# Kernel optimization log

Measured on AMD Instinct MI355X. Metric: run time of the kernel, lower is better.

Reference implementation:

```python
import jax, jax.numpy as jnp
import numpy as np
from jax import lax


def setup_inputs() -> dict:
    key = jax.random.key(0)
    kx, kk = jax.random.split(key)
    B, H, W, Cin, Cout, K = 32, 128, 128, 128, 128, 3
    X = jax.random.normal(kx, (B, H, W, Cin), dtype=jnp.float32)
    kernel = jax.random.normal(kk, (B, K, K, Cin, Cout), dtype=jnp.float32)
    return {"X": X, "kernel": kernel}


def reference(X, kernel):
    """Per-sample dynamic conv2d: each batch element gets its own HWIO kernel.

    Equivalent math to the TF depthwise-trick + reduce_sum, but expressed as a
    vmapped standard convolution (fuses the input-channel reduction, avoiding
    the huge [H',W',B*Cin,Cout] intermediate). Padding = 'VALID'.
    """
    dn = ('NHWC', 'HWIO', 'NHWC')

    def conv_one(x, k):
        # x: [H, W, Cin], k: [kh, kw, Cin, Cout] -> [H', W', Cout]
        return lax.conv_general_dilated(
            x[None], k, window_strides=(1, 1), padding='VALID',
            dimension_numbers=dn)[0]

    return jax.vmap(conv_one)(X, kernel)  # [B, H', W', Cout]
```

## Files before the change

### kernel.cpp

```cpp
#include <hip/hip_runtime.h>
#include <stdint.h>

typedef __attribute__((ext_vector_type(8))) short bf16x8;
typedef __attribute__((ext_vector_type(4))) float f32x4;
typedef __attribute__((ext_vector_type(4))) unsigned short u16x4;
typedef __attribute__((ext_vector_type(4))) unsigned int u32x4;

#define NB 32
#define HH 128
#define WW 128
#define CI 128
#define CO 128
#define HO 126
#define WO 126
#define TH 16
#define TW 16
#define PHh 18
#define PWw 18
#define NROW (PHh * PWw)
#define RSTR 72
#define RSTRB 144

__device__ __forceinline__ unsigned short f2bf(float f) {
  union { float f; unsigned u; } x; x.f = f;
  unsigned u = x.u;
  u += 0x7FFFu + ((u >> 16) & 1u);
  return (unsigned short)(u >> 16);
}

__device__ __forceinline__ unsigned cvtpk_bf16(float a, float b) {
  unsigned r;
  asm("v_cvt_pk_bf16_f32 %0, %1, %2" : "=v"(r) : "v"(a), "v"(b));
  return r;
}

__global__ void prep_kt(const float* __restrict__ kin, unsigned short* __restrict__ ktr) {
  __shared__ unsigned short t[CI * CO];
  int bp = blockIdx.x;
  int b = bp / 9, p = bp % 9;
  const float* src = kin + (size_t)bp * (CI * CO);
  unsigned short* dstb = ktr + (size_t)b * (9 * CI * CO);
  for (int i = threadIdx.x; i < CI * CO / 4; i += blockDim.x) {
    f32x4 v = *(const f32x4*)(src + i * 4);
    u16x4 o;
    o.x = f2bf(v.x); o.y = f2bf(v.y); o.z = f2bf(v.z); o.w = f2bf(v.w);
    *(u16x4*)&t[i * 4] = o;
  }
  __syncthreads();
  for (int j = threadIdx.x; j < 2048; j += blockDim.x) {
    int lane = j & 63, f = (j >> 6) & 7, sl = j >> 9;
    int ch = sl >> 1, kc = sl & 1;
    int co = (f >> 2) * 64 + (f & 3) * 16 + (lane & 15);
    int ci0 = ch * 64 + kc * 32 + (lane >> 4) * 8;
    bf16x8 v;
#pragma unroll
    for (int e = 0; e < 8; ++e) v[e] = t[(ci0 + e) * CO + co];
    int slice = (ch * 9 + p) * 2 + kc;
    *(bf16x8*)&dstb[(size_t)slice * 4096 + f * 512 + lane * 8] = v;
  }
}

__global__ void conv_naive(const float* __restrict__ X, const float* __restrict__ Kf,
                           float* __restrict__ out) {
  int idx = blockIdx.x * blockDim.x + threadIdx.x;
  if (idx >= NB * HO * WO * CO) return;
  int co = idx & 127, t = idx >> 7;
  int wp = t % WO; t /= WO;
  int hp = t % HO; int b = t / HO;
  const float* xb = X + (size_t)b * HH * WW * CI;
  const float* kb = Kf + (size_t)b * 9 * CI * CO;
  float s = 0.f;
  for (int p = 0; p < 9; ++p) {
    int kh = p / 3, kw = p % 3;
    const float* xr = xb + ((size_t)(hp + kh) * WW + (wp + kw)) * CI;
    const float* kr = kb + (size_t)p * CI * CO + co;
    for (int ci = 0; ci < CI; ++ci) s += xr[ci] * kr[(size_t)ci * CO];
  }
  out[idx] = s;
}

__global__ __launch_bounds__(512, 2) void conv_main(
    const float* __restrict__ X, const unsigned short* __restrict__ Kt,
    float* __restrict__ out) {
  __shared__ unsigned short lds_a[2][NROW * RSTR];

  const int tid = threadIdx.x;
  const int lane = tid & 63;
  const int wid = tid >> 6;
  const int wr = wid >> 2, wc = wid & 3;
  const int ks = lane >> 4, lr = lane & 15;

  const int bx = blockIdx.x;
  const int xcd = bx & 7, v = bx >> 3;
  const int b = xcd * 4 + (v >> 3);
  const int wt = v & 7;
  const int w0 = wt * TW;

  const float* xb = X + (size_t)b * HH * WW * CI;

  const int ci8 = tid & 7;
  unsigned okw = 0;
  int hI[6]; unsigned baseI[6];
#pragma unroll
  for (int i = 0; i < 6; ++i) {
    int row = (tid >> 3) + 64 * i;
    int h = row / PWw, w = row - PWw * h;
    int gw = w0 + w;
    if (gw < WW) okw |= (1u << i);
    hI[i] = h;
    baseI[i] = (unsigned)((h * WW + (gw & 127)) * CI + ci8 * 8);
  }
  const int dst0 = (tid >> 3) * RSTR + ci8 * 8;

  auto sIssue = [&](int i, int h0n, int chn, f32x4& ga, f32x4& gb) {
    bool live = (i < 5) | (tid < 32);
    bool ok = live && ((okw >> i) & 1) && (h0n + hI[i] < HH);
    const float* sp = xb + (ok ? baseI[i] + (unsigned)(h0n << 14) + (unsigned)(chn << 6)
                               : (unsigned)(ci8 << 3));
    ga = *(const f32x4*)sp;
    gb = *(const f32x4*)(sp + 4);
  };
  auto sWrite = [&](int i, int h0n, unsigned short* wbuf, const f32x4& ga, const f32x4& gb) {
    bool live = (i < 5) | (tid < 32);
    if (!live) return;
    bool ok = ((okw >> i) & 1) && (h0n + hI[i] < HH);
    u32x4 o;
    o.x = ok ? cvtpk_bf16(ga.x, ga.y) : 0u;
    o.y = ok ? cvtpk_bf16(ga.z, ga.w) : 0u;
    o.z = ok ? cvtpk_bf16(gb.x, gb.y) : 0u;
    o.w = ok ? cvtpk_bf16(gb.z, gb.w) : 0u;
    *(u32x4*)&wbuf[dst0 + i * 4608] = o;
  };

  const int aoff = ((wr * 8) * PWw + lr) * RSTRB + ks * 16;

  const unsigned short* ktw = Kt + (size_t)b * 9 * CI * CO + (wc * 2) * 512 + lane * 8;
  bf16x8 Hf[3][2];
  auto loadB = [&](bf16x8 (&dst)[2], const unsigned short* p) {
#pragma unroll
    for (int n = 0; n < 2; ++n)
      dst[n] = *(const bf16x8*)(p + n * 512);
  };

  f32x4 zero = {0.f, 0.f, 0.f, 0.f};
  f32x4 acc[8][2];
#pragma unroll
  for (int m = 0; m < 8; ++m)
#pragma unroll
    for (int n = 0; n < 2; ++n) acc[m][n] = zero;

  unsigned short* const A0 = &lds_a[0][0];
  unsigned short* const A1 = &lds_a[1][0];
  float* const ob = out + (size_t)b * HO * WO * CO;

  {
    f32x4 a0, b0, a1, b1, a2, b2;
    sIssue(0, 0, 0, a0, b0); sIssue(1, 0, 0, a1, b1); sIssue(2, 0, 0, a2, b2);
    sWrite(0, 0, A0, a0, b0); sWrite(1, 0, A0, a1, b1); sWrite(2, 0, A0, a2, b2);
    sIssue(3, 0, 0, a0, b0); sIssue(4, 0, 0, a1, b1); sIssue(5, 0, 0, a2, b2);
    sWrite(3, 0, A0, a0, b0); sWrite(4, 0, A0, a1, b1); sWrite(5, 0, A0, a2, b2);
  }
  loadB(Hf[0], ktw);
  loadB(Hf[1], ktw + 4096);
  __syncthreads();

  f32x4 g0a, g0b, g1a, g1b, g2a, g2b;

#pragma unroll 1
  for (int k = 0; k < 16; ++k) {
    const int ch = k & 1;
    const int h0 = (k >> 1) * TH;
    unsigned short* rbuf = ch ? A1 : A0;
    unsigned short* wbuf = ch ? A0 : A1;
    const unsigned short* bq = ktw + (size_t)ch * 73728;
    const bool stg = (k < 15);
    const int chn = (k + 1) & 1;
    const int h0n = ((k + 1) >> 1) * TH;
    const unsigned short* bqn = ktw + (size_t)chn * 73728;
    const char* rb = (const char*)rbuf;

#pragma unroll
    for (int s = 0; s < 18; ++s) {
      if (s < 16) loadB(Hf[(s + 2) % 3], bq + (size_t)(s + 2) * 4096);
      else if (stg) loadB(Hf[(s + 2) % 3], bqn + (size_t)(s - 16) * 4096);
      if (stg && s == 0) {
        sIssue(0, h0n, chn, g0a, g0b);
        sIssue(1, h0n, chn, g1a, g1b);
        sIssue(2, h0n, chn, g2a, g2b);
      }
      {
        const int kh = s / 6, jj = s % 6;
        const int kw = jj >> 1, kc = jj & 1;
        bf16x8 af[8];
#pragma unroll
        for (int m = 0; m < 8; ++m)
          af[m] = *(const bf16x8*)(rb + aoff +
                                   ((m + kh) * PWw * RSTRB + kw * RSTRB + kc * 64));
        __builtin_amdgcn_s_setprio(1);
#pragma unroll
        for (int m = 0; m < 8; ++m)
#pragma unroll
          for (int n = 0; n < 2; ++n)
            acc[m][n] = __builtin_amdgcn_mfma_f32_16x16x32_bf16(af[m], Hf[s % 3][n],
                                                                acc[m][n], 0, 0, 0);
        __builtin_amdgcn_s_setprio(0);
      }
      if (stg && s == 5) {
        sWrite(0, h0n, wbuf, g0a, g0b);
        sWrite(1, h0n, wbuf, g1a, g1b);
        sWrite(2, h0n, wbuf, g2a, g2b);
        sIssue(3, h0n, chn, g0a, g0b);
        sIssue(4, h0n, chn, g1a, g1b);
        sIssue(5, h0n, chn, g2a, g2b);
      }
      if (stg && s == 11) {
        sWrite(3, h0n, wbuf, g0a, g0b);
        sWrite(4, h0n, wbuf, g1a, g1b);
        sWrite(5, h0n, wbuf, g2a, g2b);
      }
    }

    if (ch) {
#pragma unroll
      for (int m = 0; m < 8; ++m) {
        int hp = h0 + wr * 8 + m;
        if (hp >= HO) continue;
#pragma unroll
        for (int r = 0; r < 4; ++r) {
          int wp = w0 + ks * 4 + r;
          if (wp >= WO) continue;
#pragma unroll
          for (int n = 0; n < 2; ++n) {
            int co = wc * 32 + n * 16 + lr;
            ob[((size_t)hp * WO + wp) * CO + co] = acc[m][n][r];
          }
        }
      }
#pragma unroll
      for (int m = 0; m < 8; ++m)
#pragma unroll
        for (int n = 0; n < 2; ++n) acc[m][n] = zero;
    }
    if (k < 15) __syncthreads();
  }
}

extern "C" void kernel_launch(void* const* d_in, const int* in_sizes, int n_in,
                              void* d_out, int out_size, void* d_ws, size_t ws_size,
                              hipStream_t stream) {
  const float* X = (const float*)d_in[0];
  const float* Kf = (const float*)d_in[1];
  float* out = (float*)d_out;
  size_t need = (size_t)NB * 9 * CI * CO * sizeof(unsigned short);
  if (d_ws != nullptr && ws_size >= need) {
    unsigned short* ktr = (unsigned short*)d_ws;
    prep_kt<<<dim3(NB * 9), 256, 0, stream>>>(Kf, ktr);
    conv_main<<<dim3(256), 512, 0, stream>>>(X, ktr, out);
  } else {
    int total = NB * HO * WO * CO;
    conv_naive<<<(total + 255) / 256, 256, 0, stream>>>(X, Kf, out);
  }
}
```

Before: 178.2 us.

## Enlarge row tile to 21 with 12 waves per block and re-pipeline staging

```diff
diff --git a/kernel.cpp b/kernel.cpp
--- a/kernel.cpp
+++ b/kernel.cpp
@@ -13,11 +13,11 @@
 #define CO 128
 #define HO 126
 #define WO 126
-#define TH 16
+#define TH3 21
 #define TW 16
-#define PHh 18
+#define PH3 23
 #define PWw 18
-#define NROW (PHh * PWw)
+#define NR3 (PH3 * PWw)
 #define RSTR 72
 #define RSTRB 144
 
@@ -79,10 +79,10 @@
   out[idx] = s;
 }
 
-__global__ __launch_bounds__(512, 2) void conv_main(
+__global__ __launch_bounds__(768, 3) void conv_main(
     const float* __restrict__ X, const unsigned short* __restrict__ Kt,
     float* __restrict__ out) {
-  __shared__ unsigned short lds_a[2][NROW * RSTR];
+  __shared__ unsigned short lds_a[2][NR3 * RSTR];
 
   const int tid = threadIdx.x;
   const int lane = tid & 63;
@@ -99,131 +99,120 @@
   const float* xb = X + (size_t)b * HH * WW * CI;
 
   const int ci8 = tid & 7;
-  unsigned okw = 0;
-  int hI[6]; unsigned baseI[6];
-#pragma unroll
-  for (int i = 0; i < 6; ++i) {
-    int row = (tid >> 3) + 64 * i;
-    int h = row / PWw, w = row - PWw * h;
-    int gw = w0 + w;
-    if (gw < WW) okw |= (1u << i);
-    hI[i] = h;
-    baseI[i] = (unsigned)((h * WW + (gw & 127)) * CI + ci8 * 8);
-  }
-  const int dst0 = (tid >> 3) * RSTR + ci8 * 8;
-
-  auto sIssue = [&](int i, int h0n, int chn, f32x4& ga, f32x4& gb) {
-    bool live = (i < 5) | (tid < 32);
-    bool ok = live && ((okw >> i) & 1) && (h0n + hI[i] < HH);
-    const float* sp = xb + (ok ? baseI[i] + (unsigned)(h0n << 14) + (unsigned)(chn << 6)
-                               : (unsigned)(ci8 << 3));
-    ga = *(const f32x4*)sp;
-    gb = *(const f32x4*)(sp + 4);
+  const int row0 = tid >> 3;
+  const int h00 = row0 / PWw, w00 = row0 - PWw * h00;
+  const int dst0 = row0 * RSTR + ci8 * 8;
+
+  const int aoff = ((wr * 7) * PWw + lr) * RSTRB + ks * 16;
+
+  const unsigned short* ktw = Kt + (size_t)b * 9 * CI * CO + (wc * 2) * 512 + lane * 8;
+  bf16x8 Hf[2][2];
+  auto loadB = [&](bf16x8 (&dst)[2], const unsigned short* p) {
+    dst[0] = *(const bf16x8*)(p);
+    dst[1] = *(const bf16x8*)(p + 512);
   };
-  auto sWrite = [&](int i, int h0n, unsigned short* wbuf, const f32x4& ga, const f32x4& gb) {
-    bool live = (i < 5) | (tid < 32);
-    if (!live) return;
-    bool ok = ((okw >> i) & 1) && (h0n + hI[i] < HH);
-    u32x4 o;
-    o.x = ok ? cvtpk_bf16(ga.x, ga.y) : 0u;
-    o.y = ok ? cvtpk_bf16(ga.z, ga.w) : 0u;
-    o.z = ok ? cvtpk_bf16(gb.x, gb.y) : 0u;
-    o.w = ok ? cvtpk_bf16(gb.z, gb.w) : 0u;
-    *(u32x4*)&wbuf[dst0 + i * 4608] = o;
-  };
-
-  const int aoff = ((wr * 8) * PWw + lr) * RSTRB + ks * 16;
-
-  const unsigned short* ktw = Kt + (size_t)b * 9 * CI * CO + (wc * 2) * 512 + lane * 8;
-  bf16x8 Hf[3][2];
-  auto loadB = [&](bf16x8 (&dst)[2], const unsigned short* p) {
-#pragma unroll
-    for (int n = 0; n < 2; ++n)
-      dst[n] = *(const bf16x8*)(p + n * 512);
-  };
 
   f32x4 zero = {0.f, 0.f, 0.f, 0.f};
-  f32x4 acc[8][2];
-#pragma unroll
-  for (int m = 0; m < 8; ++m)
+  f32x4 acc[7][2];
+#pragma unroll
+  for (int m = 0; m < 7; ++m)
 #pragma unroll
     for (int n = 0; n < 2; ++n) acc[m][n] = zero;
 
-  unsigned short* const A0 = &lds_a[0][0];
-  unsigned short* const A1 = &lds_a[1][0];
   float* const ob = out + (size_t)b * HO * WO * CO;
 
   {
-    f32x4 a0, b0, a1, b1, a2, b2;
-    sIssue(0, 0, 0, a0, b0); sIssue(1, 0, 0, a1, b1); sIssue(2, 0, 0, a2, b2);
-    sWrite(0, 0, A0, a0, b0); sWrite(1, 0, A0, a1, b1); sWrite(2, 0, A0, a2, b2);
-    sIssue(3, 0, 0, a0, b0); sIssue(4, 0, 0, a1, b1); sIssue(5, 0, 0, a2, b2);
-    sWrite(3, 0, A0, a0, b0); sWrite(4, 0, A0, a1, b1); sWrite(5, 0, A0, a2, b2);
+    int hC = h00, wC = w00;
+#pragma unroll
+    for (int g = 0; g < 5; ++g) {
+      bool live = (g < 4) | (tid < 240);
+      int gh = hC, gw = w0 + wC;
+      bool ok = live && ((gh | gw) < HH);
+      const float* sp = xb + ((size_t)(((gh & 127) << 7) + (gw & 127)) << 7) + ci8 * 8;
+      f32x4 ga = *(const f32x4*)sp;
+      f32x4 gb = *(const f32x4*)(sp + 4);
+      if (live) {
+        u32x4 o;
+        o.x = ok ? cvtpk_bf16(ga.x, ga.y) : 0u;
+        o.y = ok ? cvtpk_bf16(ga.z, ga.w) : 0u;
+        o.z = ok ? cvtpk_bf16(gb.x, gb.y) : 0u;
+        o.w = ok ? cvtpk_bf16(gb.z, gb.w) : 0u;
+        *(u32x4*)&lds_a[0][dst0 + g * 6912] = o;
+      }
+      wC += 6; if (wC >= PWw) { wC -= PWw; hC += 6; } else hC += 5;
+    }
   }
   loadB(Hf[0], ktw);
-  loadB(Hf[1], ktw + 4096);
   __syncthreads();
 
-  f32x4 g0a, g0b, g1a, g1b, g2a, g2b;
+  f32x4 gAa, gAb, gBa, gBb; bool okA = false, okB = false;
+  int hC = h00, wC = w00;
 
 #pragma unroll 1
-  for (int k = 0; k < 16; ++k) {
-    const int ch = k & 1;
-    const int h0 = (k >> 1) * TH;
-    unsigned short* rbuf = ch ? A1 : A0;
-    unsigned short* wbuf = ch ? A0 : A1;
+  for (int kp = 0; kp < 12; ++kp) {
+    const int ch = kp & 1;
+    const int h0 = (kp >> 1) * TH3;
+    const char* rb = (const char*)&lds_a[kp & 1][0];
+    unsigned short* wbuf = &lds_a[(kp + 1) & 1][0];
     const unsigned short* bq = ktw + (size_t)ch * 73728;
-    const bool stg = (k < 15);
-    const int chn = (k + 1) & 1;
-    const int h0n = ((k + 1) >> 1) * TH;
+    const bool stg = (kp < 11);
+    const int chn = (kp + 1) & 1;
+    const int h0n = ((kp + 1) >> 1) * TH3;
     const unsigned short* bqn = ktw + (size_t)chn * 73728;
-    const char* rb = (const char*)rbuf;
+    if (stg) { hC = h00; wC = w00; }
 
 #pragma unroll
     for (int s = 0; s < 18; ++s) {
-      if (s < 16) loadB(Hf[(s + 2) % 3], bq + (size_t)(s + 2) * 4096);
-      else if (stg) loadB(Hf[(s + 2) % 3], bqn + (size_t)(s - 16) * 4096);
-      if (stg && s == 0) {
-        sIssue(0, h0n, chn, g0a, g0b);
-        sIssue(1, h0n, chn, g1a, g1b);
-        sIssue(2, h0n, chn, g2a, g2b);
+      const int kh = s / 6, jj = s % 6;
+      const int kw = jj >> 1, kc = jj & 1;
+      if (s < 17) loadB(Hf[(s + 1) & 1], bq + (size_t)(s + 1) * 4096);
+      else if (stg) loadB(Hf[0], bqn);
+      if (stg && s >= 2 && s < 7) {
+        const int g = s - 2;
+        bool live = (g < 4) | (tid < 240);
+        if (live) {
+          bool ok = (g & 1) ? okB : okA;
+          f32x4 ga = (g & 1) ? gBa : gAa;
+          f32x4 gb = (g & 1) ? gBb : gAb;
+          u32x4 o;
+          o.x = ok ? cvtpk_bf16(ga.x, ga.y) : 0u;
+          o.y = ok ? cvtpk_bf16(ga.z, ga.w) : 0u;
+          o.z = ok ? cvtpk_bf16(gb.x, gb.y) : 0u;
+          o.w = ok ? cvtpk_bf16(gb.z, gb.w) : 0u;
+          *(u32x4*)&wbuf[dst0 + g * 6912] = o;
+        }
+      }
+      if (stg && s < 5) {
+        bool live = (s < 4) | (tid < 240);
+        int gh = h0n + hC, gw = w0 + wC;
+        bool ok = live && ((gh | gw) < HH);
+        const float* sp = xb + ((size_t)(((gh & 127) << 7) + (gw & 127)) << 7)
+                          + chn * 64 + ci8 * 8;
+        if (s & 1) { gBa = *(const f32x4*)sp; gBb = *(const f32x4*)(sp + 4); okB = ok; }
+        else       { gAa = *(const f32x4*)sp; gAb = *(const f32x4*)(sp + 4); okA = ok; }
+        wC += 6; if (wC >= PWw) { wC -= PWw; hC += 6; } else hC += 5;
       }
       {
-        const int kh = s / 6, jj = s % 6;
-        const int kw = jj >> 1, kc = jj & 1;
-        bf16x8 af[8];
-#pragma unroll
-        for (int m = 0; m < 8; ++m)
+        bf16x8 af[7];
+#pragma unroll
+        for (int m = 0; m < 7; ++m)
           af[m] = *(const bf16x8*)(rb + aoff +
-                                   ((m + kh) * PWw * RSTRB + kw * RSTRB + kc * 64));
+                                   (((m + kh) * PWw + kw) * RSTRB + kc * 64));
         __builtin_amdgcn_s_setprio(1);
 #pragma unroll
-        for (int m = 0; m < 8; ++m)
+        for (int m = 0; m < 7; ++m)
 #pragma unroll
           for (int n = 0; n < 2; ++n)
-            acc[m][n] = __builtin_amdgcn_mfma_f32_16x16x32_bf16(af[m], Hf[s % 3][n],
+            acc[m][n] = __builtin_amdgcn_mfma_f32_16x16x32_bf16(af[m], Hf[s & 1][n],
                                                                 acc[m][n], 0, 0, 0);
         __builtin_amdgcn_s_setprio(0);
       }
-      if (stg && s == 5) {
-        sWrite(0, h0n, wbuf, g0a, g0b);
-        sWrite(1, h0n, wbuf, g1a, g1b);
-        sWrite(2, h0n, wbuf, g2a, g2b);
-        sIssue(3, h0n, chn, g0a, g0b);
-        sIssue(4, h0n, chn, g1a, g1b);
-        sIssue(5, h0n, chn, g2a, g2b);
-      }
-      if (stg && s == 11) {
-        sWrite(3, h0n, wbuf, g0a, g0b);
-        sWrite(4, h0n, wbuf, g1a, g1b);
-        sWrite(5, h0n, wbuf, g2a, g2b);
-      }
     }
 
     if (ch) {
 #pragma unroll
-      for (int m = 0; m < 8; ++m) {
-        int hp = h0 + wr * 8 + m;
+      for (int m = 0; m < 7; ++m) {
+        int hp = h0 + wr * 7 + m;
         if (hp >= HO) continue;
 #pragma unroll
         for (int r = 0; r < 4; ++r) {
@@ -237,11 +226,11 @@
         }
       }
 #pragma unroll
-      for (int m = 0; m < 8; ++m)
+      for (int m = 0; m < 7; ++m)
 #pragma unroll
         for (int n = 0; n < 2; ++n) acc[m][n] = zero;
     }
-    if (k < 15) __syncthreads();
+    if (kp < 11) __syncthreads();
   }
 }
 
@@ -255,7 +244,7 @@
   if (d_ws != nullptr && ws_size >= need) {
     unsigned short* ktr = (unsigned short*)d_ws;
     prep_kt<<<dim3(NB * 9), 256, 0, stream>>>(Kf, ktr);
-    conv_main<<<dim3(256), 512, 0, stream>>>(X, ktr, out);
+    conv_main<<<dim3(256), 768, 0, stream>>>(X, ktr, out);
   } else {
     int total = NB * HO * WO * CO;
     conv_naive<<<(total + 255) / 256, 256, 0, stream>>>(X, Kf, out);
```

New measurement: 470.4 us. 2.64x slower.
